# Kernel tuning notes

Measured on AMD Instinct MI355X. Metric: run time of the kernel, lower is better.

The kernel has to match this reference:

```python
import jax, jax.numpy as jnp
import numpy as np

WINDOW_SIZE = 5
CONSISTENCY_WEIGHT = 1.0


def _wsum(x, w):
    # sliding-window sum along axis 1 via exclusive cumsum differences
    s = jnp.cumsum(x, axis=1)
    s = jnp.pad(s, ((0, 0), (1, 0)))
    return s[:, w:] - s[:, :-w]  # [B, L-w+1]


def setup_inputs() -> dict:
    key = jax.random.key(0)
    k1, k2, k3 = jax.random.split(key, 3)
    B, L, C = 512, 16384, 2
    return {
        "predictions": jax.random.normal(k1, (B, L, C), dtype=jnp.float32),
        "targets": jax.random.randint(k2, (B, L), 0, 2, dtype=jnp.int32),
        "mask": jax.random.randint(k3, (B, L), 0, 2, dtype=jnp.int32),
    }


def reference(predictions, targets, mask):
    w = WINDOW_SIZE
    probs = jax.nn.softmax(predictions, axis=-1)[..., 1]  # [B, L]
    t = targets.astype(jnp.float32)
    m = mask.astype(jnp.float32)

    msum = _wsum(m, w)                       # [B, W]
    denom = jnp.maximum(msum, 1.0)           # clamp(min=1.0)
    spm = _wsum(probs * m, w)
    stm = _wsum(t * m, w)
    sp2m = _wsum(probs * probs * m, w)
    st2m = _wsum(t * t * m, w)

    pmean = spm / denom
    tmean = stm / denom
    # masked biased variance: sum((x - mean)^2 * m) / clamp(msum, 1)
    pvar = (sp2m - 2.0 * pmean * spm + pmean * pmean * msum) / denom
    tvar = (st2m - 2.0 * tmean * stm + tmean * tmean * msum) / denom

    mse = jnp.mean((pvar - tvar) ** 2, axis=0)          # per-window MSE over batch, [W]
    valid = (jnp.sum(msum, axis=0) > 0).astype(jnp.float32)  # skip windows with zero mask
    cnt = jnp.maximum(jnp.sum(valid), 1.0)
    loss = jnp.sum(mse * valid) / cnt * CONSISTENCY_WEIGHT
    return loss
```

## Files before the change

### kernel.cpp

```cpp
#include <hip/hip_runtime.h>
#include <math.h>

#define BATCH 512
#define LEN   16384
#define WIN   5
#define WOUT  (LEN - WIN + 1)
#define TPB   256
#define WPT   4
#define WPB   (TPB * WPT)
#define EPT   (WPT + WIN - 1)
#define WBLKS ((WOUT + WPB - 1) / WPB)
#define RWGS  ((WOUT + TPB - 1) / TPB)
#define NCH2  16

#define LBUF   19456
#define MT_ISS 5
#define PR_ISS 9
#define N_ISS  (2 * MT_ISS + PR_ISS)

__device__ __forceinline__ float fast_rcp(float x) {
    float r = __builtin_amdgcn_rcpf(x);
    return r * fmaf(-x, r, 2.0f);
}

struct RowRaw {
    int4   m0, m1, t0, t1;
    float4 q0, q1, q2, q3;
};
struct RowArr {
    float m[EPT], tm[EPT], pm[EPT], p2m[EPT];
};

__device__ __forceinline__ RowArr convert_row(const RowRaw& r) {
    RowArr a;
    const int mi[EPT] = {r.m0.x, r.m0.y, r.m0.z, r.m0.w,
                         r.m1.x, r.m1.y, r.m1.z, r.m1.w};
    const int ti[EPT] = {r.t0.x, r.t0.y, r.t0.z, r.t0.w,
                         r.t1.x, r.t1.y, r.t1.z, r.t1.w};
    const float dx[EPT] = {r.q0.x - r.q0.y, r.q0.z - r.q0.w,
                           r.q1.x - r.q1.y, r.q1.z - r.q1.w,
                           r.q2.x - r.q2.y, r.q2.z - r.q2.w,
                           r.q3.x - r.q3.y, r.q3.z - r.q3.w};
#pragma unroll
    for (int i = 0; i < EPT; ++i) {
        const float p  = fast_rcp(1.0f + __expf(dx[i]));
        const float mf = (float)mi[i];
        a.m[i]   = mf;
        a.tm[i]  = (float)(ti[i] & mi[i]);
        a.pm[i]  = p * mf;
        a.p2m[i] = p * p * mf;
    }
    return a;
}

__device__ __forceinline__ void windows_row(const RowArr& a,
                                            float accd2[WPT], float accms[WPT]) {
#pragma unroll
    for (int w = 0; w < WPT; ++w) {
        float msum = 0.f, stm = 0.f, spm = 0.f, sp2m = 0.f;
#pragma unroll
        for (int k = 0; k < WIN; ++k) {
            msum += a.m[w + k];
            stm  += a.tm[w + k];
            spm  += a.pm[w + k];
            sp2m += a.p2m[w + k];
        }
        const float denom = fmaxf(msum, 1.0f);
        const float inv   = fast_rcp(denom);
        const float pmean = spm * inv;
        const float tmean = stm * inv;
        const float pvar  = (sp2m - 2.0f * pmean * spm + pmean * pmean * msum) * inv;
        const float tvar  = (stm  - 2.0f * tmean * stm + tmean * tmean * msum) * inv;
        const float d = pvar - tvar;
        accd2[w] += d * d;
        accms[w] += msum;
    }
}

__global__ __launch_bounds__(TPB)
void bcl_partial_staged(const float* __restrict__ pred,
                        const int*   __restrict__ tgt,
                        const int*   __restrict__ msk,
                        float* __restrict__ part_d2,
                        float* __restrict__ part_ms,
                        int bper) {
    __shared__ __align__(1024) char s_lds[2 * LBUF];
    const int col   = blockIdx.x;
    const int chunk = blockIdx.y;
    const int tid   = (int)threadIdx.x;
    const int lane  = tid & 63, wid = tid >> 6;
    const int j0    = col * WPB + tid * WPT;
    const int b0    = chunk * bper;

    const char* mbytes = (const char*)msk;
    const char* tbytes = (const char*)tgt;
    const char* pbytes = (const char*)pred;
    const int cmt = col * (WPB * 4);
    const int cpr = col * (WPB * 8);

    auto stage = [&](char* buf, int b) {
        const char* mrow = mbytes + (size_t)b * (LEN * 4);
        const char* trow = tbytes + (size_t)b * (LEN * 4);
        const char* prow = pbytes + (size_t)b * (LEN * 8);
        for (int i = wid; i < N_ISS; i += 4) {
            const char* src; char* dst;
            if (i < MT_ISS) {
                int off = cmt + (i << 10);
                if (off > LEN * 4 - 1024) off = LEN * 4 - 1024;
                src = mrow + off;  dst = buf + (i << 10);
            } else if (i < 2 * MT_ISS) {
                const int k = i - MT_ISS;
                int off = cmt + (k << 10);
                if (off > LEN * 4 - 1024) off = LEN * 4 - 1024;
                src = trow + off;  dst = buf + 5120 + (k << 10);
            } else {
                const int k = i - 2 * MT_ISS;
                int off = cpr + (k << 10);
                if (off > LEN * 8 - 1024) off = LEN * 8 - 1024;
                src = prow + off;  dst = buf + 10240 + (k << 10);
            }
            __builtin_amdgcn_global_load_lds(
                (const __attribute__((address_space(1))) unsigned int*)(src + lane * 16),
                (__attribute__((address_space(3))) unsigned int*)dst,
                16, 0, 0);
        }
    };

    char* cur = s_lds;
    char* nxt = s_lds + LBUF;

    float accd2[WPT] = {0.f, 0.f, 0.f, 0.f};
    float accms[WPT] = {0.f, 0.f, 0.f, 0.f};

    stage(cur, b0);
    asm volatile("s_waitcnt vmcnt(0)" ::: "memory");
    __syncthreads();

    for (int it = 0; it < bper; ++it) {
        if (it + 1 < bper) stage(nxt, b0 + it + 1);

        if (j0 < WOUT) {
            RowRaw r;
            const int e0 = tid << 4;
            r.m0 = *(const int4*)(cur + e0);
            r.m1 = *(const int4*)(cur + e0 + 16);
            r.t0 = *(const int4*)(cur + 5120 + e0);
            r.t1 = *(const int4*)(cur + 5120 + e0 + 16);
            const int p0 = 10240 + (tid << 5);
            r.q0 = *(const float4*)(cur + p0);
            r.q1 = *(const float4*)(cur + p0 + 16);
            r.q2 = *(const float4*)(cur + p0 + 32);
            r.q3 = *(const float4*)(cur + p0 + 48);
            RowArr a = convert_row(r);
            windows_row(a, accd2, accms);
        }

        asm volatile("s_waitcnt vmcnt(0)" ::: "memory");
        __syncthreads();
        char* t = cur; cur = nxt; nxt = t;
    }

    if (j0 < WOUT) {
        *(float4*)(part_d2 + (size_t)chunk * WOUT + j0) =
            make_float4(accd2[0], accd2[1], accd2[2], accd2[3]);
        *(float4*)(part_ms + (size_t)chunk * WOUT + j0) =
            make_float4(accms[0], accms[1], accms[2], accms[3]);
    }
}

__global__ __launch_bounds__(TPB)
void bcl_chunk_reduce(const float* __restrict__ part_d2,
                      const float* __restrict__ part_ms,
                      float* __restrict__ p2_d2,
                      float* __restrict__ p2_ms,
                      double* __restrict__ accum,
                      unsigned int* __restrict__ ticket,
                      int rf) {
    if (blockIdx.x == 0 && blockIdx.y == 0 && threadIdx.x == 0) {
        accum[0] = 0.0; accum[1] = 0.0; *ticket = 0u;
    }
    const int j = blockIdx.x * blockDim.x + threadIdx.x;
    if (j >= WOUT) return;
    const int c0 = blockIdx.y * rf;
    float d2 = 0.f, ms = 0.f;
#pragma unroll 8
    for (int c = c0; c < c0 + rf; ++c) {
        d2 += part_d2[(size_t)c * WOUT + j];
        ms += part_ms[(size_t)c * WOUT + j];
    }
    p2_d2[(size_t)blockIdx.y * WOUT + j] = d2;
    p2_ms[(size_t)blockIdx.y * WOUT + j] = ms;
}

__global__ __launch_bounds__(TPB)
void bcl_window_reduce(const float* __restrict__ p2_d2,
                       const float* __restrict__ p2_ms,
                       double* __restrict__ accum,
                       unsigned int* __restrict__ ticket,
                       float* __restrict__ out,
                       int nch2) {
    const int j = blockIdx.x * blockDim.x + threadIdx.x;
    double num = 0.0, cnt = 0.0;
    if (j < WOUT) {
        float d2 = 0.f, ms = 0.f;
#pragma unroll 8
        for (int c = 0; c < nch2; ++c) {
            d2 += p2_d2[(size_t)c * WOUT + j];
            ms += p2_ms[(size_t)c * WOUT + j];
        }
        if (ms > 0.f) {
            num = (double)d2 * (1.0 / (double)BATCH);
            cnt = 1.0;
        }
    }
    for (int off = 32; off > 0; off >>= 1) {
        num += __shfl_down(num, off, 64);
        cnt += __shfl_down(cnt, off, 64);
    }
    __shared__ double s_num[4], s_cnt[4];
    const int lane = threadIdx.x & 63, wave = threadIdx.x >> 6;
    if (lane == 0) { s_num[wave] = num; s_cnt[wave] = cnt; }
    __syncthreads();
    if (threadIdx.x == 0) {
        double n = 0.0, c = 0.0;
        for (int wv = 0; wv < TPB / 64; ++wv) { n += s_num[wv]; c += s_cnt[wv]; }
        atomicAdd(&accum[0], n);
        atomicAdd(&accum[1], c);
        __threadfence();
        const unsigned int t = atomicAdd(ticket, 1u);
        if (t == gridDim.x - 1) {
            out[0] = (float)(accum[0] / fmax(accum[1], 1.0));
        }
    }
}

extern "C" void kernel_launch(void* const* d_in, const int* in_sizes, int n_in,
                              void* d_out, int out_size, void* d_ws, size_t ws_size,
                              hipStream_t stream) {
    const float* pred = (const float*)d_in[0];
    const int*   tgt  = (const int*)d_in[1];
    const int*   msk  = (const int*)d_in[2];
    float* out = (float*)d_out;

    int nchunks = 128;
    while (nchunks > 2) {
        size_t need = (size_t)(nchunks + NCH2) * WOUT * 2 * sizeof(float) + 256;
        if (need <= ws_size) break;
        nchunks >>= 1;
    }
    const int bper = BATCH / nchunks;
    const int nch2 = (nchunks >= NCH2) ? NCH2 : nchunks;
    const int rf   = nchunks / nch2;

    float* part_d2 = (float*)d_ws;
    float* part_ms = part_d2 + (size_t)nchunks * WOUT;
    float* p2_d2   = part_ms + (size_t)nchunks * WOUT;
    float* p2_ms   = p2_d2   + (size_t)NCH2 * WOUT;
    size_t off = ((size_t)((char*)(p2_ms + (size_t)NCH2 * WOUT) - (char*)d_ws) + 15) & ~(size_t)15;
    double* accum = (double*)((char*)d_ws + off);
    unsigned int* ticket = (unsigned int*)(accum + 2);

    dim3 g1(WBLKS, nchunks);
    bcl_partial_staged<<<g1, TPB, 0, stream>>>(pred, tgt, msk, part_d2, part_ms, bper);

    dim3 gA(RWGS, nch2);
    bcl_chunk_reduce<<<gA, TPB, 0, stream>>>(part_d2, part_ms, p2_d2, p2_ms,
                                             accum, ticket, rf);

    bcl_window_reduce<<<RWGS, TPB, 0, stream>>>(p2_d2, p2_ms, accum, ticket, out, nch2);
}
```

Measured before the change: 167.2 us.

## Drop intermediate chunk-reduce kernel and cut batch chunks to reduce partial traffic

Cuts the number of batch chunks in the main partial kernel from 128 to 32 and removes the middle reduction kernel, so the final window reduce sums all chunk partials directly. Accumulator and ticket initialization moves into the first kernel. This removes one kernel launch and shrinks the partial-sum buffers written and read back. In exchange, each block of the main kernel handles more batch rows, so the grid has fewer blocks and less parallelism to hide load latency.

```diff
diff --git a/kernel.cpp b/kernel.cpp
--- a/kernel.cpp
+++ b/kernel.cpp
@@ -11,7 +11,6 @@
 #define EPT   (WPT + WIN - 1)
 #define WBLKS ((WOUT + WPB - 1) / WPB)
 #define RWGS  ((WOUT + TPB - 1) / TPB)
-#define NCH2  16
 
 #define LBUF   19456
 #define MT_ISS 5
@@ -83,6 +82,8 @@
                         const int*   __restrict__ msk,
                         float* __restrict__ part_d2,
                         float* __restrict__ part_ms,
+                        double* __restrict__ accum,
+                        unsigned int* __restrict__ ticket,
                         int bper) {
     __shared__ __align__(1024) char s_lds[2 * LBUF];
     const int col   = blockIdx.x;
@@ -91,6 +92,10 @@
     const int lane  = tid & 63, wid = tid >> 6;
     const int j0    = col * WPB + tid * WPT;
     const int b0    = chunk * bper;
+
+    if (col == 0 && chunk == 0 && tid == 0) {
+        accum[0] = 0.0; accum[1] = 0.0; *ticket = 0u;
+    }
 
     const char* mbytes = (const char*)msk;
     const char* tbytes = (const char*)tgt;
@@ -169,44 +174,20 @@
 }
 
 __global__ __launch_bounds__(TPB)
-void bcl_chunk_reduce(const float* __restrict__ part_d2,
-                      const float* __restrict__ part_ms,
-                      float* __restrict__ p2_d2,
-                      float* __restrict__ p2_ms,
-                      double* __restrict__ accum,
-                      unsigned int* __restrict__ ticket,
-                      int rf) {
-    if (blockIdx.x == 0 && blockIdx.y == 0 && threadIdx.x == 0) {
-        accum[0] = 0.0; accum[1] = 0.0; *ticket = 0u;
-    }
-    const int j = blockIdx.x * blockDim.x + threadIdx.x;
-    if (j >= WOUT) return;
-    const int c0 = blockIdx.y * rf;
-    float d2 = 0.f, ms = 0.f;
-#pragma unroll 8
-    for (int c = c0; c < c0 + rf; ++c) {
-        d2 += part_d2[(size_t)c * WOUT + j];
-        ms += part_ms[(size_t)c * WOUT + j];
-    }
-    p2_d2[(size_t)blockIdx.y * WOUT + j] = d2;
-    p2_ms[(size_t)blockIdx.y * WOUT + j] = ms;
-}
-
-__global__ __launch_bounds__(TPB)
-void bcl_window_reduce(const float* __restrict__ p2_d2,
-                       const float* __restrict__ p2_ms,
+void bcl_window_reduce(const float* __restrict__ part_d2,
+                       const float* __restrict__ part_ms,
                        double* __restrict__ accum,
                        unsigned int* __restrict__ ticket,
                        float* __restrict__ out,
-                       int nch2) {
+                       int nchunks) {
     const int j = blockIdx.x * blockDim.x + threadIdx.x;
     double num = 0.0, cnt = 0.0;
     if (j < WOUT) {
         float d2 = 0.f, ms = 0.f;
 #pragma unroll 8
-        for (int c = 0; c < nch2; ++c) {
-            d2 += p2_d2[(size_t)c * WOUT + j];
-            ms += p2_ms[(size_t)c * WOUT + j];
+        for (int c = 0; c < nchunks; ++c) {
+            d2 += part_d2[(size_t)c * WOUT + j];
+            ms += part_ms[(size_t)c * WOUT + j];
         }
         if (ms > 0.f) {
             num = (double)d2 * (1.0 / (double)BATCH);
@@ -242,30 +223,24 @@
     const int*   msk  = (const int*)d_in[2];
     float* out = (float*)d_out;
 
-    int nchunks = 128;
+    int nchunks = 32;
     while (nchunks > 2) {
-        size_t need = (size_t)(nchunks + NCH2) * WOUT * 2 * sizeof(float) + 256;
+        size_t need = (size_t)nchunks * WOUT * 2 * sizeof(float) + 256;
         if (need <= ws_size) break;
         nchunks >>= 1;
     }
     const int bper = BATCH / nchunks;
-    const int nch2 = (nchunks >= NCH2) ? NCH2 : nchunks;
-    const int rf   = nchunks / nch2;
 
     float* part_d2 = (float*)d_ws;
     float* part_ms = part_d2 + (size_t)nchunks * WOUT;
-    float* p2_d2   = part_ms + (size_t)nchunks * WOUT;
-    float* p2_ms   = p2_d2   + (size_t)NCH2 * WOUT;
-    size_t off = ((size_t)((char*)(p2_ms + (size_t)NCH2 * WOUT) - (char*)d_ws) + 15) & ~(size_t)15;
+    size_t off = ((size_t)((char*)(part_ms + (size_t)nchunks * WOUT) - (char*)d_ws) + 15) & ~(size_t)15;
     double* accum = (double*)((char*)d_ws + off);
     unsigned int* ticket = (unsigned int*)(accum + 2);
 
     dim3 g1(WBLKS, nchunks);
-    bcl_partial_staged<<<g1, TPB, 0, stream>>>(pred, tgt, msk, part_d2, part_ms, bper);
-
-    dim3 gA(RWGS, nch2);
-    bcl_chunk_reduce<<<gA, TPB, 0, stream>>>(part_d2, part_ms, p2_d2, p2_ms,
-                                             accum, ticket, rf);
-
-    bcl_window_reduce<<<RWGS, TPB, 0, stream>>>(p2_d2, p2_ms, accum, ticket, out, nch2);
-}
+    bcl_partial_staged<<<g1, TPB, 0, stream>>>(pred, tgt, msk, part_d2, part_ms,
+                                               accum, ticket, bper);
+
+    bcl_window_reduce<<<RWGS, TPB, 0, stream>>>(part_d2, part_ms, accum, ticket,
+                                                out, nchunks);
+}
```

Measured after the change: 158.0 us. 1.06x faster.
